# Kernel tuning notes

Hardware: AMD Instinct MI355X
Metric: run time of the kernel (lower is better)

Reference implementation:

```python
import jax, jax.numpy as jnp
import numpy as np

B, TQ, TKV, D_MODEL, H, DQ, DV = 4, 2048, 2048, 1024, 16, 64, 64
DK = DQ

def setup_inputs() -> dict:
    key = jax.random.key(0)
    ks = jax.random.split(key, 8)
    s = 0.02
    return {
        "query_sequence": jax.random.normal(ks[0], (B, TQ, D_MODEL), jnp.float32),
        "key_value_sequence": jax.random.normal(ks[1], (B, TKV, D_MODEL), jnp.float32),
        "key_value_padding_mask": jnp.zeros((B, TKV), dtype=bool),
        "Wq": jax.random.normal(ks[2], (D_MODEL, H * DQ), jnp.float32) * s,
        "bq": jnp.zeros((H * DQ,), jnp.float32),
        "Wkv": jax.random.normal(ks[3], (D_MODEL, H * (DK + DV)), jnp.float32) * s,
        "bkv": jnp.zeros((H * (DK + DV),), jnp.float32),
        "Wo": jax.random.normal(ks[4], (H * DV, D_MODEL), jnp.float32) * s,
        "bo": jnp.zeros((D_MODEL,), jnp.float32),
        "apply_causal_mask": 1,
    }

def reference(query_sequence, key_value_sequence, key_value_padding_mask,
              Wq, bq, Wkv, bkv, Wo, bo, apply_causal_mask):
    b, tq, _ = query_sequence.shape
    tkv = key_value_sequence.shape[1]
    q = (query_sequence @ Wq + bq).reshape(b, tq, H, DQ)          # (B,Tq,H,Dq)
    kv = key_value_sequence @ Wkv + bkv
    k = kv[..., : H * DK].reshape(b, tkv, H, DK)                   # (B,Tkv,H,Dk)
    v = kv[..., H * DK :].reshape(b, tkv, H, DV)                   # (B,Tkv,H,Dv)
    scores = jnp.einsum("bqhd,bkhd->bhqk", q, k) / jnp.sqrt(jnp.float32(DK))
    neg_inf = jnp.float32(-jnp.inf)
    scores = jnp.where(key_value_padding_mask[:, None, None, :], neg_inf, scores)
    if apply_causal_mask:
        causal = jnp.tril(jnp.ones((tq, tkv), dtype=bool))
        scores = jnp.where(causal[None, None, :, :], scores, neg_inf)
    attn = jax.nn.softmax(scores, axis=-1)
    out = jnp.einsum("bhqk,bkhd->bqhd", attn, v).reshape(b, tq, H * DV)
    return out @ Wo + bo
```

## Files before the change

kernel.cpp:

```cpp
#include <hip/hip_runtime.h>
#include <hip/hip_bf16.h>

#define B_   4
#define TQ_  2048
#define TKV_ 2048
#define DM_  1024
#define H_   16
#define DH_  64

#define SC_FOLD 0.18033688011112042f

using f32x4  = __attribute__((ext_vector_type(4))) float;
using f32x16 = __attribute__((ext_vector_type(16))) float;
using s16x8  = __attribute__((ext_vector_type(8))) short;

static __device__ __forceinline__ unsigned short f2bf(float f) {
  union { float f; unsigned int u; } v; v.f = f;
  unsigned int r = v.u + 0x7FFFu + ((v.u >> 16) & 1u);
  return (unsigned short)(r >> 16);
}
static __device__ __forceinline__ unsigned int pk2(float a, float b) {
  unsigned int r;
  asm("v_cvt_pk_bf16_f32 %0, %1, %2" : "=v"(r) : "v"(a), "v"(b));
  return r;
}
static __device__ __forceinline__ float max3f(float a, float b, float c) {
  float r;
  asm("v_max3_f32 %0, %1, %2, %3" : "=v"(r) : "v"(a), "v"(b), "v"(c));
  return r;
}

#define GL16(g, l)                                                          \
  __builtin_amdgcn_global_load_lds(                                         \
      (const __attribute__((address_space(1))) unsigned int*)(g),           \
      (__attribute__((address_space(3))) unsigned int*)(l), 16, 0, 0)

__global__ __launch_bounds__(256) void k_transpose_cast_all(
    const float* __restrict__ Wq, unsigned short* __restrict__ WqT,
    const float* __restrict__ Wkv, unsigned short* __restrict__ WkvT,
    const float* __restrict__ Wo, unsigned short* __restrict__ WoT) {
  __shared__ float t[64][65];
  int bid = blockIdx.x;
  const float* W;
  unsigned short* WT;
  int K = 1024, N, n0, k0;
  float scale;
  if (bid < 256) {
    W = Wq; WT = WqT; N = 1024; scale = SC_FOLD;
    n0 = (bid & 15) * 64; k0 = (bid >> 4) * 64;
  } else if (bid < 768) {
    int b2 = bid - 256;
    W = Wkv; WT = WkvT; N = 2048; scale = 1.0f;
    n0 = (b2 & 31) * 64; k0 = (b2 >> 5) * 64;
  } else {
    int b2 = bid - 768;
    W = Wo; WT = WoT; N = 1024; scale = 1.0f;
    n0 = (b2 & 15) * 64; k0 = (b2 >> 4) * 64;
  }
  int tx = threadIdx.x & 63, ty = threadIdx.x >> 6;
#pragma unroll
  for (int i = 0; i < 64; i += 4)
    t[ty + i][tx] = W[(size_t)(k0 + ty + i) * N + n0 + tx];
  __syncthreads();
#pragma unroll
  for (int i = 0; i < 64; i += 4)
    WT[(size_t)(n0 + ty + i) * K + k0 + tx] = f2bf(t[tx][ty + i] * scale);
}

__global__ __launch_bounds__(256) void k_cast_bf16(
    const float* __restrict__ in, unsigned short* __restrict__ out, int n4) {
  for (int i = blockIdx.x * 256 + threadIdx.x; i < n4; i += gridDim.x * 256) {
    f32x4 v = *(const f32x4*)(in + (size_t)i * 4);
    unsigned long long u = (unsigned long long)pk2(v[0], v[1]) |
                           ((unsigned long long)pk2(v[2], v[3]) << 32);
    *(unsigned long long*)(out + (size_t)i * 4) = u;
  }
}

template <int MODE, int BN>
__global__ __launch_bounds__(512, 2) void k_gemm8(
    const unsigned short* __restrict__ A, const unsigned short* __restrict__ BT,
    const float* __restrict__ bias, float bscale, unsigned short* __restrict__ out_a,
    unsigned short* __restrict__ out_b, float* __restrict__ out_f, int Kd) {
  constexpr int NI = BN / 64;
  constexpr int NH = NI / 2;
  __shared__ __align__(16) unsigned short As[2 * 256 * 64];
  __shared__ __align__(16) unsigned short Bs[2 * BN * 64];
  const int tid = threadIdx.x, lane = tid & 63, w = tid >> 6;
  const int wm = w >> 2, wn = w & 3;

  int nwg = gridDim.x * gridDim.y;
  int bid = blockIdx.y * gridDim.x + blockIdx.x;
  int cpx = nwg >> 3;
  int sw = (bid & 7) * cpx + (bid >> 3);
  int bx = sw % gridDim.x, by = sw / gridDim.x;
  int m0 = by * 256, n0 = bx * BN;

  const int strow = tid >> 3;
  const int sx = ((tid & 7) << 4) ^ ((strow & 7) << 4);
  const char* gA = (const char*)(A + (size_t)(m0 + strow) * Kd) + sx;
  const char* gB = (const char*)(BT + (size_t)(n0 + strow) * Kd) + sx;
  char* lA = (char*)As;
  char* lB = (char*)Bs;

#define ST_A(bf, c, k0) \
  GL16(gA + ((size_t)(c) * 64 * Kd + (size_t)(k0)) * 2, lA + (bf) * 32768 + (c) * 8192 + tid * 16)
#define ST_B(bf, c, k0) \
  GL16(gB + ((size_t)(c) * 64 * Kd + (size_t)(k0)) * 2, lB + (bf) * (BN * 128) + (c) * 8192 + tid * 16)

  f32x4 acc[8][NI];
#pragma unroll
  for (int i = 0; i < 8; ++i)
#pragma unroll
    for (int j = 0; j < NI; ++j) acc[i][j] = (f32x4){0.f, 0.f, 0.f, 0.f};

  s16x8 afr[4][2], bfr[NI][2];
  const int arow = wm * 128 + (lane & 15);
  const int brow = wn * (NI * 16) + (lane & 15);
  const int fcol = (lane >> 4) * 16;

#define RD_A(bf, r) (*(const s16x8*)(lA + (bf) * 32768 + (r) * 128 + ((fcol + _kk * 64) ^ (((r) & 7) << 4))))
#define RD_B(bf, r) (*(const s16x8*)(lB + (bf) * (BN * 128) + (r) * 128 + ((fcol + _kk * 64) ^ (((r) & 7) << 4))))

  const int nT = Kd >> 6;

  ST_B(0, 0, 0); ST_B(0, 1, 0);
  if (BN == 256) { ST_B(0, 2, 0); ST_B(0, 3, 0); }
  ST_A(0, 0, 0); ST_A(0, 2, 0);
  ST_A(0, 1, 0); ST_A(0, 3, 0);
  asm volatile("s_waitcnt vmcnt(2)" ::: "memory");
  __builtin_amdgcn_s_barrier();

#pragma unroll 1
  for (int t = 0; t < nT; ++t) {
    const int cur = t & 1, nxt = cur ^ 1;
    const int k1 = (t + 1) << 6;
    const bool st = (t + 1 < nT);

#pragma unroll
    for (int mi = 0; mi < 4; ++mi)
#pragma unroll
      for (int _kk = 0; _kk < 2; ++_kk) afr[mi][_kk] = RD_A(cur, arow + mi * 16);
#pragma unroll
    for (int ni = 0; ni < NH; ++ni)
#pragma unroll
      for (int _kk = 0; _kk < 2; ++_kk) bfr[ni][_kk] = RD_B(cur, brow + ni * 16);
    if (st) { ST_B(nxt, 0, k1); ST_B(nxt, 1, k1); }
    __builtin_amdgcn_s_barrier();
    __builtin_amdgcn_s_setprio(1);
#pragma unroll
    for (int mi = 0; mi < 4; ++mi)
#pragma unroll
      for (int ni = 0; ni < NH; ++ni)
#pragma unroll
        for (int kk = 0; kk < 2; ++kk)
          acc[mi][ni] = __builtin_amdgcn_mfma_f32_16x16x32_bf16(afr[mi][kk], bfr[ni][kk], acc[mi][ni], 0, 0, 0);
    __builtin_amdgcn_s_setprio(0);
    __builtin_amdgcn_s_barrier();

#pragma unroll
    for (int ni = NH; ni < NI; ++ni)
#pragma unroll
      for (int _kk = 0; _kk < 2; ++_kk) bfr[ni][_kk] = RD_B(cur, brow + ni * 16);
    if (st) {
      if (BN == 256) { ST_B(nxt, 2, k1); ST_B(nxt, 3, k1); }
      else           { ST_A(nxt, 0, k1); ST_A(nxt, 2, k1); }
    }
    if (st) asm volatile("s_waitcnt vmcnt(4)" ::: "memory");
    else    asm volatile("s_waitcnt vmcnt(0)" ::: "memory");
    __builtin_amdgcn_s_barrier();
    __builtin_amdgcn_s_setprio(1);
#pragma unroll
    for (int mi = 0; mi < 4; ++mi)
#pragma unroll
      for (int ni = NH; ni < NI; ++ni)
#pragma unroll
        for (int kk = 0; kk < 2; ++kk)
          acc[mi][ni] = __builtin_amdgcn_mfma_f32_16x16x32_bf16(afr[mi][kk], bfr[ni][kk], acc[mi][ni], 0, 0, 0);
    __builtin_amdgcn_s_setprio(0);
    __builtin_amdgcn_s_barrier();

#pragma unroll
    for (int mi = 0; mi < 4; ++mi)
#pragma unroll
      for (int _kk = 0; _kk < 2; ++_kk) afr[mi][_kk] = RD_A(cur, arow + (mi + 4) * 16);
    if (st) {
      if (BN == 256) { ST_A(nxt, 0, k1); ST_A(nxt, 2, k1); }
      else           { ST_A(nxt, 1, k1); ST_A(nxt, 3, k1); }
    }
    __builtin_amdgcn_s_barrier();
    __builtin_amdgcn_s_setprio(1);
#pragma unroll
    for (int mi = 0; mi < 4; ++mi)
#pragma unroll
      for (int ni = 0; ni < NH; ++ni)
#pragma unroll
        for (int kk = 0; kk < 2; ++kk)
          acc[mi + 4][ni] = __builtin_amdgcn_mfma_f32_16x16x32_bf16(afr[mi][kk], bfr[ni][kk], acc[mi + 4][ni], 0, 0, 0);
    __builtin_amdgcn_s_setprio(0);
    __builtin_amdgcn_s_barrier();

    if (st && BN == 256) { ST_A(nxt, 1, k1); ST_A(nxt, 3, k1); }
    asm volatile("s_waitcnt vmcnt(2)" ::: "memory");
    __builtin_amdgcn_s_barrier();
    __builtin_amdgcn_s_setprio(1);
#pragma unroll
    for (int mi = 0; mi < 4; ++mi)
#pragma unroll
      for (int ni = NH; ni < NI; ++ni)
#pragma unroll
        for (int kk = 0; kk < 2; ++kk)
          acc[mi + 4][ni] = __builtin_amdgcn_mfma_f32_16x16x32_bf16(afr[mi][kk], bfr[ni][kk], acc[mi + 4][ni], 0, 0, 0);
    __builtin_amdgcn_s_setprio(0);
    __builtin_amdgcn_s_barrier();
  }

#pragma unroll
  for (int mi = 0; mi < 8; ++mi) {
#pragma unroll
    for (int ni = 0; ni < NI; ++ni) {
      int col = n0 + wn * (NI * 16) + ni * 16 + (lane & 15);
      int rbase = m0 + wm * 128 + mi * 16 + (lane >> 4) * 4;
      float bv = bias[col] * bscale;
      if (MODE == 1 && col >= H_ * DH_) {
        int c2 = col - H_ * DH_;
        int h = c2 >> 6, d = c2 & 63;
        int b = rbase >> 11, tt = rbase & 2047;
        union { unsigned short h4[4]; unsigned long long u; } p;
#pragma unroll
        for (int r = 0; r < 4; ++r) p.h4[r] = f2bf(acc[mi][ni][r] + bv);
        *(unsigned long long*)(out_b + ((((size_t)b * H_ + h) * DH_ + d) * TKV_ + tt)) = p.u;
      } else {
#pragma unroll
        for (int r = 0; r < 4; ++r) {
          float v = acc[mi][ni][r] + bv;
          int m = rbase + r;
          if (MODE == 0) {
            int b = m >> 11, tt = m & 2047;
            int h = col >> 6, d = col & 63;
            out_a[(((size_t)b * H_ + h) * TQ_ + tt) * DH_ + d] = f2bf(v);
          } else if (MODE == 1) {
            int b = m >> 11, tt = m & 2047;
            int h = col >> 6, d = col & 63;
            out_a[(((size_t)b * H_ + h) * TKV_ + tt) * DH_ + d] = f2bf(v);
          } else {
            out_f[(size_t)m * DM_ + col] = v;
          }
        }
      }
    }
  }
#undef ST_A
#undef ST_B
#undef RD_A
#undef RD_B
}

__global__ __launch_bounds__(256, 2) void k_attn(
    const unsigned short* __restrict__ Qb, const unsigned short* __restrict__ Kb,
    const unsigned short* __restrict__ Vtb, const unsigned char* __restrict__ mask,
    const int* __restrict__ cflag, unsigned short* __restrict__ Ob) {
  __shared__ __align__(16) unsigned short Kt[2][128 * 64];
  __shared__ __align__(16) unsigned short Vt[2][64 * 128];
  __shared__ float bias_lds[2][128];
  __shared__ float red[4][32];
  __shared__ int s_any;

  int bid = blockIdx.y * gridDim.x + blockIdx.x;
  int r8 = bid & 7, q8 = bid >> 3;
  int bh = r8 * 8 + (q8 >> 3);
  int bx = q8 & 7;

  int b = bh >> 4, h = bh & 15;
  int tid = threadIdx.x, lane = tid & 63, w = tid >> 6;
  int hi = lane >> 5, l31 = lane & 31, l7 = lane & 7;
  const unsigned short* Qp = Qb + (size_t)bh * TQ_ * DH_;
  const char* Kp = (const char*)(Kb + (size_t)bh * TKV_ * DH_);
  const char* Vp = (const char*)(Vtb + (size_t)bh * DH_ * TKV_);
  const unsigned char* mp = mask + (size_t)b * TKV_;
  int causal = cflag[0];

  int st_r4 = tid >> 2;
  int st_c4 = (tid & 3) * 16;
  s16x8 pKr[4], pVr[4];

#define LOAD_KV(kv0)                                                          \
  {                                                                           \
    _Pragma("unroll")                                                         \
    for (int p = 0; p < 4; ++p) {                                             \
      int krow = (p >> 1) * 64 + st_r4;                                       \
      int kx = st_c4 + (p & 1) * 64;                                          \
      pKr[p] = *(const s16x8*)(Kp + ((size_t)((kv0) + krow) * 128 + kx));     \
      int vx = st_c4 + p * 64;                                                \
      pVr[p] = *(const s16x8*)(Vp + (((size_t)st_r4 * TKV_ + (kv0)) * 2 + vx)); \
    }                                                                         \
  }
#define WRITE_KV(bufi)                                                        \
  {                                                                           \
    char* kb_ = (char*)&Kt[bufi][0];                                          \
    char* vb_ = (char*)&Vt[bufi][0];                                          \
    _Pragma("unroll")                                                         \
    for (int p = 0; p < 4; ++p) {                                             \
      int krow = (p >> 1) * 64 + st_r4;                                       \
      int kx = st_c4 + (p & 1) * 64;                                          \
      *(s16x8*)(kb_ + krow * 128 + (kx ^ ((st_r4 & 7) << 4))) = pKr[p];       \
      int vx = st_c4 + p * 64;                                                \
      *(s16x8*)(vb_ + st_r4 * 256 + (vx ^ ((st_r4 & 7) << 4))) = pVr[p];      \
    }                                                                         \
  }

  if (tid == 0) s_any = 0;
  __syncthreads();
  {
    int any = 0;
    for (int i = tid; i < TKV_; i += 256) any |= mp[i];
    if (any) s_any = 1;
  }
  __syncthreads();
  const int has_mask = s_any;

#pragma unroll 1
  for (int pass = 0; pass < 2; ++pass) {
    int qb = (pass ? (15 - bx) : bx) * 128;
    int qw = qb + w * 32;
    int qrow = qw + l31;

    s16x8 bQ[4];
#pragma unroll
    for (int kk = 0; kk < 4; ++kk)
      bQ[kk] = *(const s16x8*)(Qp + (size_t)qrow * DH_ + kk * 16 + hi * 8);

    f32x16 accO[2];
#pragma unroll
    for (int i = 0; i < 16; ++i) { accO[0][i] = 0.f; accO[1][i] = 0.f; }
    float m_run = -INFINITY, l_run = 0.f;

    int nT = (causal ? (qb + 128) : TKV_) >> 7;

    LOAD_KV(0);
    WRITE_KV(0);
    if (has_mask && tid < 128) bias_lds[0][tid] = mp[tid] ? -1e30f : 0.0f;
    __syncthreads();

#pragma unroll 1
    for (int it = 0; it < nT; ++it) {
      int kv0 = it << 7;
      int cur = it & 1, nxt = cur ^ 1;
      if (it + 1 < nT) LOAD_KV(kv0 + 128);

      char* kbase = (char*)&Kt[cur][0];
      char* vbase = (char*)&Vt[cur][0];

      int nact = 4;
      if (causal) {
        int rem = qw + 31 - kv0;
        nact = rem < 0 ? 0 : ((rem >> 5) + 1);
        if (nact > 4) nact = 4;
      }

      if (nact > 0) {
        f32x16 sT[4];
        __builtin_amdgcn_s_setprio(1);
#pragma unroll
        for (int s = 0; s < 4; ++s) {
          if (s < nact) {
#pragma unroll
            for (int i = 0; i < 16; ++i) sT[s][i] = 0.f;
#pragma unroll
            for (int kk = 0; kk < 4; ++kk) {
              s16x8 aK = *(const s16x8*)(kbase + (s * 32 + l31) * 128 +
                                         ((kk * 32 + hi * 16) ^ (l7 << 4)));
              sT[s] = __builtin_amdgcn_mfma_f32_32x32x16_bf16(aK, bQ[kk], sT[s], 0, 0, 0);
            }
          }
        }
        __builtin_amdgcn_s_setprio(0);

        float a0 = -INFINITY, a1 = -INFINITY, a2 = -INFINITY, a3 = -INFINITY;
#pragma unroll
        for (int s = 0; s < 4; ++s) {
          if (s < nact) {
            int diag_s = causal && (kv0 + s * 32 + 31 > qw);
            if (diag_s || has_mask) {
#pragma unroll
              for (int r = 0; r < 16; ++r) {
                int kvloc = s * 32 + (r & 3) + 8 * (r >> 2) + 4 * hi;
                float sv = sT[s][r];
                if (has_mask) sv += bias_lds[cur][kvloc];
                if (diag_s && (kv0 + kvloc) > qrow) sv = -1e30f;
                sT[s][r] = sv;
              }
            }
#pragma unroll
            for (int r = 0; r < 16; r += 4) {
              a0 = fmaxf(a0, sT[s][r + 0]); a1 = fmaxf(a1, sT[s][r + 1]);
              a2 = fmaxf(a2, sT[s][r + 2]); a3 = fmaxf(a3, sT[s][r + 3]);
            }
          }
        }
        float mx = max3f(max3f(a0, a1, a2), a3, -3.0e30f);
        mx = fmaxf(mx, __shfl_xor(mx, 32));

        if (!__all(mx - m_run <= 8.0f)) {
          float mnew = fmaxf(m_run, mx);
          float sc_o = exp2f(m_run - mnew);
          m_run = mnew;
          l_run *= sc_o;
          red[w][l31] = sc_o;
#pragma unroll
          for (int r = 0; r < 16; ++r) {
            float f = red[w][(r & 3) + 8 * (r >> 2) + 4 * hi];
            accO[0][r] *= f;
            accO[1][r] *= f;
          }
        }

        float s0acc = 0.f, s1acc = 0.f, s2acc = 0.f, s3acc = 0.f;
#pragma unroll
        for (int s = 0; s < 4; ++s) {
          if (s < nact) {
#pragma unroll
            for (int r = 0; r < 16; r += 4) {
              float p0 = exp2f(sT[s][r + 0] - m_run);
              float p1 = exp2f(sT[s][r + 1] - m_run);
              float p2 = exp2f(sT[s][r + 2] - m_run);
              float p3 = exp2f(sT[s][r + 3] - m_run);
              sT[s][r + 0] = p0; sT[s][r + 1] = p1;
              sT[s][r + 2] = p2; sT[s][r + 3] = p3;
              s0acc += p0; s1acc += p1; s2acc += p2; s3acc += p3;
            }
          }
        }
        float ls = (s0acc + s1acc) + (s2acc + s3acc);
        ls += __shfl_xor(ls, 32);
        l_run += ls;

#pragma unroll
        for (int c = 0; c < 8; ++c) {
          if ((c >> 1) < nact) {
            int s = c >> 1, kk = c & 1;
            unsigned int x0 = pk2(sT[s][8 * kk + 0], sT[s][8 * kk + 1]);
            unsigned int y0 = pk2(sT[s][8 * kk + 2], sT[s][8 * kk + 3]);
            unsigned int x1 = pk2(sT[s][8 * kk + 4], sT[s][8 * kk + 5]);
            unsigned int y1 = pk2(sT[s][8 * kk + 6], sT[s][8 * kk + 7]);
            asm("v_permlane32_swap_b32 %0, %1" : "+v"(x0), "+v"(x1));
            asm("v_permlane32_swap_b32 %0, %1" : "+v"(y0), "+v"(y1));
            union { unsigned int u[4]; s16x8 v; } pf;
            pf.u[0] = x0;
            pf.u[1] = y0;
            pf.u[2] = x1;
            pf.u[3] = y1;
            __builtin_amdgcn_s_setprio(1);
#pragma unroll
            for (int dt = 0; dt < 2; ++dt) {
              s16x8 vf = *(const s16x8*)(vbase + (dt * 32 + l31) * 256 +
                                         ((c * 32 + hi * 16) ^ (l7 << 4)));
              accO[dt] = __builtin_amdgcn_mfma_f32_32x32x16_bf16(pf.v, vf, accO[dt], 0, 0, 0);
            }
            __builtin_amdgcn_s_setprio(0);
          }
        }
      }

      if (it + 1 < nT) {
        WRITE_KV(nxt);
        if (has_mask && tid < 128) bias_lds[nxt][tid] = mp[kv0 + 128 + tid] ? -1e30f : 0.0f;
      }
      __syncthreads();
    }

    red[w][l31] = 1.0f / l_run;
#pragma unroll
    for (int r = 0; r < 16; ++r) {
      int R = (r & 3) + 8 * (r >> 2) + 4 * hi;
      float f = red[w][R];
      int qg = qw + R;
      size_t base = ((size_t)b * TQ_ + qg) * DM_ + h * DH_ + l31;
      Ob[base] = f2bf(accO[0][r] * f);
      Ob[base + 32] = f2bf(accO[1][r] * f);
    }
  }
#undef LOAD_KV
#undef WRITE_KV
}

extern "C" void kernel_launch(void* const* d_in, const int* in_sizes, int n_in,
                              void* d_out, int out_size, void* d_ws, size_t ws_size,
                              hipStream_t stream) {
  const float* xq  = (const float*)d_in[0];
  const float* xkv = (const float*)d_in[1];
  const unsigned char* mask = (const unsigned char*)d_in[2];
  const float* Wq  = (const float*)d_in[3];
  const float* bq  = (const float*)d_in[4];
  const float* Wkv = (const float*)d_in[5];
  const float* bkv = (const float*)d_in[6];
  const float* Wo  = (const float*)d_in[7];
  const float* bo  = (const float*)d_in[8];
  const int* cflag = (const int*)d_in[9];
  float* out = (float*)d_out;

  char* ws = (char*)d_ws;
  unsigned short* WqT  = (unsigned short*)(ws);
  unsigned short* WkvT = (unsigned short*)(ws + ((size_t)2 << 20));
  unsigned short* WoT  = (unsigned short*)(ws + ((size_t)6 << 20));
  unsigned short* Qb   = (unsigned short*)(ws + ((size_t)8 << 20));
  unsigned short* Kb   = (unsigned short*)(ws + ((size_t)24 << 20));
  unsigned short* Vb   = (unsigned short*)(ws + ((size_t)40 << 20));
  unsigned short* Xr   = (unsigned short*)(ws + ((size_t)56 << 20));
  unsigned short* Ob   = Xr;

  k_transpose_cast_all<<<1024, 256, 0, stream>>>(Wq, WqT, Wkv, WkvT, Wo, WoT);

  k_cast_bf16<<<2048, 256, 0, stream>>>(xq, Xr, B_ * TQ_ * DM_ / 4);
  k_gemm8<0, 128><<<dim3(8, 32), 512, 0, stream>>>(Xr, WqT, bq, SC_FOLD, Qb, nullptr, nullptr, 1024);

  k_cast_bf16<<<2048, 256, 0, stream>>>(xkv, Xr, B_ * TKV_ * DM_ / 4);
  k_gemm8<1, 256><<<dim3(8, 32), 512, 0, stream>>>(Xr, WkvT, bkv, 1.0f, Kb, Vb, nullptr, 1024);

  k_attn<<<dim3(8, B_ * H_), 256, 0, stream>>>(Qb, Kb, Vb, mask, cflag, Ob);

  k_gemm8<2, 128><<<dim3(8, 32), 512, 0, stream>>>(Ob, WoT, bo, 1.0f, nullptr, nullptr, out, 1024);
}
```

Baseline: 191.6 us.

## Widen attention blocks to 512 threads covering 256 query rows per tile

Changes the attention kernel from 4 to 8 waves per block, so each block handles 256 query rows per pass and the grid halves to 4x64 blocks. K/V tiles staged in shared memory are now shared by twice as many query rows, which halves global K/V traffic per query, and the per-thread load work is split over more threads. The trade-offs are fewer blocks in flight, coarser causal load balancing across the paired passes, and tighter launch bounds that may limit registers.

```diff
diff --git a/kernel.cpp b/kernel.cpp
--- a/kernel.cpp
+++ b/kernel.cpp
@@ -256,20 +256,20 @@
 #undef RD_B
 }
 
-__global__ __launch_bounds__(256, 2) void k_attn(
+__global__ __launch_bounds__(512, 4) void k_attn(
     const unsigned short* __restrict__ Qb, const unsigned short* __restrict__ Kb,
     const unsigned short* __restrict__ Vtb, const unsigned char* __restrict__ mask,
     const int* __restrict__ cflag, unsigned short* __restrict__ Ob) {
   __shared__ __align__(16) unsigned short Kt[2][128 * 64];
   __shared__ __align__(16) unsigned short Vt[2][64 * 128];
   __shared__ float bias_lds[2][128];
-  __shared__ float red[4][32];
+  __shared__ float red[8][32];
   __shared__ int s_any;
 
   int bid = blockIdx.y * gridDim.x + blockIdx.x;
   int r8 = bid & 7, q8 = bid >> 3;
-  int bh = r8 * 8 + (q8 >> 3);
-  int bx = q8 & 7;
+  int bh = r8 * 8 + (q8 >> 2);
+  int bx = q8 & 3;
 
   int b = bh >> 4, h = bh & 15;
   int tid = threadIdx.x, lane = tid & 63, w = tid >> 6;
@@ -280,40 +280,34 @@
   const unsigned char* mp = mask + (size_t)b * TKV_;
   int causal = cflag[0];
 
-  int st_r4 = tid >> 2;
-  int st_c4 = (tid & 3) * 16;
-  s16x8 pKr[4], pVr[4];
+  int st_kr = tid >> 2;
+  int st_kc = (tid & 3) * 16;
+  int st_vr = tid >> 3;
+  int st_vc = (tid & 7) * 16;
+  s16x8 pKr[2], pVr[2];
 
 #define LOAD_KV(kv0)                                                          \
   {                                                                           \
-    _Pragma("unroll")                                                         \
-    for (int p = 0; p < 4; ++p) {                                             \
-      int krow = (p >> 1) * 64 + st_r4;                                       \
-      int kx = st_c4 + (p & 1) * 64;                                          \
-      pKr[p] = *(const s16x8*)(Kp + ((size_t)((kv0) + krow) * 128 + kx));     \
-      int vx = st_c4 + p * 64;                                                \
-      pVr[p] = *(const s16x8*)(Vp + (((size_t)st_r4 * TKV_ + (kv0)) * 2 + vx)); \
-    }                                                                         \
+    pKr[0] = *(const s16x8*)(Kp + ((size_t)((kv0) + st_kr) * 128 + st_kc));   \
+    pKr[1] = *(const s16x8*)(Kp + ((size_t)((kv0) + st_kr) * 128 + st_kc + 64)); \
+    pVr[0] = *(const s16x8*)(Vp + (((size_t)st_vr * TKV_ + (kv0)) * 2 + st_vc)); \
+    pVr[1] = *(const s16x8*)(Vp + (((size_t)st_vr * TKV_ + (kv0)) * 2 + st_vc + 128)); \
   }
 #define WRITE_KV(bufi)                                                        \
   {                                                                           \
     char* kb_ = (char*)&Kt[bufi][0];                                          \
     char* vb_ = (char*)&Vt[bufi][0];                                          \
-    _Pragma("unroll")                                                         \
-    for (int p = 0; p < 4; ++p) {                                             \
-      int krow = (p >> 1) * 64 + st_r4;                                       \
-      int kx = st_c4 + (p & 1) * 64;                                          \
-      *(s16x8*)(kb_ + krow * 128 + (kx ^ ((st_r4 & 7) << 4))) = pKr[p];       \
-      int vx = st_c4 + p * 64;                                                \
-      *(s16x8*)(vb_ + st_r4 * 256 + (vx ^ ((st_r4 & 7) << 4))) = pVr[p];      \
-    }                                                                         \
+    *(s16x8*)(kb_ + st_kr * 128 + (st_kc ^ ((st_kr & 7) << 4))) = pKr[0];     \
+    *(s16x8*)(kb_ + st_kr * 128 + ((st_kc + 64) ^ ((st_kr & 7) << 4))) = pKr[1]; \
+    *(s16x8*)(vb_ + st_vr * 256 + (st_vc ^ ((st_vr & 7) << 4))) = pVr[0];     \
+    *(s16x8*)(vb_ + st_vr * 256 + ((st_vc + 128) ^ ((st_vr & 7) << 4))) = pVr[1]; \
   }
 
   if (tid == 0) s_any = 0;
   __syncthreads();
   {
     int any = 0;
-    for (int i = tid; i < TKV_; i += 256) any |= mp[i];
+    for (int i = tid; i < TKV_; i += 512) any |= mp[i];
     if (any) s_any = 1;
   }
   __syncthreads();
@@ -321,7 +315,7 @@
 
 #pragma unroll 1
   for (int pass = 0; pass < 2; ++pass) {
-    int qb = (pass ? (15 - bx) : bx) * 128;
+    int qb = (pass ? (7 - bx) : bx) * 256;
     int qw = qb + w * 32;
     int qrow = qw + l31;
 
@@ -335,7 +329,7 @@
     for (int i = 0; i < 16; ++i) { accO[0][i] = 0.f; accO[1][i] = 0.f; }
     float m_run = -INFINITY, l_run = 0.f;
 
-    int nT = (causal ? (qb + 128) : TKV_) >> 7;
+    int nT = (causal ? (qb + 256) : TKV_) >> 7;
 
     LOAD_KV(0);
     WRITE_KV(0);
@@ -517,7 +511,7 @@
   k_cast_bf16<<<2048, 256, 0, stream>>>(xkv, Xr, B_ * TKV_ * DM_ / 4);
   k_gemm8<1, 256><<<dim3(8, 32), 512, 0, stream>>>(Xr, WkvT, bkv, 1.0f, Kb, Vb, nullptr, 1024);
 
-  k_attn<<<dim3(8, B_ * H_), 256, 0, stream>>>(Qb, Kb, Vb, mask, cflag, Ob);
+  k_attn<<<dim3(4, B_ * H_), 512, 0, stream>>>(Qb, Kb, Vb, mask, cflag, Ob);
 
   k_gemm8<2, 128><<<dim3(8, 32), 512, 0, stream>>>(Ob, WoT, bo, 1.0f, nullptr, nullptr, out, 1024);
 }
```

Measured after the change: 355.1 us. 1.85x slower.

## Merge weight prep with input casts and fuse Q and KV projection GEMMs

Applied to the files above, without the earlier changes.

Merges the weight transposes and both activation casts into one prep kernel, and runs the Q and KV projection GEMMs as a single launch with 512 workgroups. This removes launch gaps and serialization between small kernels and lets the Q and KV GEMMs share the GPU at once. KV activations need a separate workspace region, so the fused path only runs when the workspace is large enough; otherwise it falls back to separate launches. The fused GEMM reserves LDS sized for BN=256 even for Q blocks, which could change occupancy.

```diff
diff --git a/kernel.cpp b/kernel.cpp
--- a/kernel.cpp
+++ b/kernel.cpp
@@ -35,28 +35,9 @@
       (const __attribute__((address_space(1))) unsigned int*)(g),           \
       (__attribute__((address_space(3))) unsigned int*)(l), 16, 0, 0)
 
-__global__ __launch_bounds__(256) void k_transpose_cast_all(
-    const float* __restrict__ Wq, unsigned short* __restrict__ WqT,
-    const float* __restrict__ Wkv, unsigned short* __restrict__ WkvT,
-    const float* __restrict__ Wo, unsigned short* __restrict__ WoT) {
-  __shared__ float t[64][65];
-  int bid = blockIdx.x;
-  const float* W;
-  unsigned short* WT;
-  int K = 1024, N, n0, k0;
-  float scale;
-  if (bid < 256) {
-    W = Wq; WT = WqT; N = 1024; scale = SC_FOLD;
-    n0 = (bid & 15) * 64; k0 = (bid >> 4) * 64;
-  } else if (bid < 768) {
-    int b2 = bid - 256;
-    W = Wkv; WT = WkvT; N = 2048; scale = 1.0f;
-    n0 = (b2 & 31) * 64; k0 = (b2 >> 5) * 64;
-  } else {
-    int b2 = bid - 768;
-    W = Wo; WT = WoT; N = 1024; scale = 1.0f;
-    n0 = (b2 & 15) * 64; k0 = (b2 >> 4) * 64;
-  }
+static __device__ __forceinline__ void transpose_tile(
+    const float* W, unsigned short* WT, int K, int N, int n0, int k0, float scale,
+    float (*t)[65]) {
   int tx = threadIdx.x & 63, ty = threadIdx.x >> 6;
 #pragma unroll
   for (int i = 0; i < 64; i += 4)
@@ -66,10 +47,9 @@
   for (int i = 0; i < 64; i += 4)
     WT[(size_t)(n0 + ty + i) * K + k0 + tx] = f2bf(t[tx][ty + i] * scale);
 }
-
-__global__ __launch_bounds__(256) void k_cast_bf16(
-    const float* __restrict__ in, unsigned short* __restrict__ out, int n4) {
-  for (int i = blockIdx.x * 256 + threadIdx.x; i < n4; i += gridDim.x * 256) {
+static __device__ __forceinline__ void cast_gs(
+    const float* in, unsigned short* out, int n4, int cb, int ncb) {
+  for (int i = cb * 256 + threadIdx.x; i < n4; i += ncb * 256) {
     f32x4 v = *(const f32x4*)(in + (size_t)i * 4);
     unsigned long long u = (unsigned long long)pk2(v[0], v[1]) |
                            ((unsigned long long)pk2(v[2], v[3]) << 32);
@@ -77,23 +57,42 @@
   }
 }
 
+__global__ __launch_bounds__(256) void k_prep(
+    const float* __restrict__ Wq, unsigned short* __restrict__ WqT,
+    const float* __restrict__ Wkv, unsigned short* __restrict__ WkvT,
+    const float* __restrict__ Wo, unsigned short* __restrict__ WoT,
+    const float* __restrict__ xq, unsigned short* __restrict__ Aq,
+    const float* __restrict__ xkv, unsigned short* __restrict__ Akv, int n4) {
+  int bid = blockIdx.x;
+  if (bid >= 3072) { cast_gs(xkv, Akv, n4, bid - 3072, 2048); return; }
+  if (bid >= 1024) { cast_gs(xq, Aq, n4, bid - 1024, 2048); return; }
+  __shared__ float t[64][65];
+  if (bid < 256) {
+    transpose_tile(Wq, WqT, 1024, 1024, (bid & 15) * 64, (bid >> 4) * 64, SC_FOLD, t);
+  } else if (bid < 768) {
+    int b2 = bid - 256;
+    transpose_tile(Wkv, WkvT, 1024, 2048, (b2 & 31) * 64, (b2 >> 5) * 64, 1.0f, t);
+  } else {
+    int b2 = bid - 768;
+    transpose_tile(Wo, WoT, 1024, 1024, (b2 & 15) * 64, (b2 >> 4) * 64, 1.0f, t);
+  }
+}
+
+__global__ __launch_bounds__(256) void k_cast_bf16(
+    const float* __restrict__ in, unsigned short* __restrict__ out, int n4) {
+  cast_gs(in, out, n4, blockIdx.x, gridDim.x);
+}
+
 template <int MODE, int BN>
-__global__ __launch_bounds__(512, 2) void k_gemm8(
+static __device__ __forceinline__ void gemm_body(
     const unsigned short* __restrict__ A, const unsigned short* __restrict__ BT,
     const float* __restrict__ bias, float bscale, unsigned short* __restrict__ out_a,
-    unsigned short* __restrict__ out_b, float* __restrict__ out_f, int Kd) {
+    unsigned short* __restrict__ out_b, float* __restrict__ out_f, int Kd,
+    int bx, int by, unsigned short* As, unsigned short* Bs) {
   constexpr int NI = BN / 64;
   constexpr int NH = NI / 2;
-  __shared__ __align__(16) unsigned short As[2 * 256 * 64];
-  __shared__ __align__(16) unsigned short Bs[2 * BN * 64];
   const int tid = threadIdx.x, lane = tid & 63, w = tid >> 6;
   const int wm = w >> 2, wn = w & 3;
-
-  int nwg = gridDim.x * gridDim.y;
-  int bid = blockIdx.y * gridDim.x + blockIdx.x;
-  int cpx = nwg >> 3;
-  int sw = (bid & 7) * cpx + (bid >> 3);
-  int bx = sw % gridDim.x, by = sw / gridDim.x;
   int m0 = by * 256, n0 = bx * BN;
 
   const int strow = tid >> 3;
@@ -256,6 +255,41 @@
 #undef RD_B
 }
 
+template <int MODE, int BN>
+__global__ __launch_bounds__(512, 2) void k_gemm8(
+    const unsigned short* __restrict__ A, const unsigned short* __restrict__ BT,
+    const float* __restrict__ bias, float bscale, unsigned short* __restrict__ out_a,
+    unsigned short* __restrict__ out_b, float* __restrict__ out_f, int Kd) {
+  __shared__ __align__(16) unsigned short As[2 * 256 * 64];
+  __shared__ __align__(16) unsigned short Bs[2 * BN * 64];
+  int nwg = gridDim.x * gridDim.y;
+  int bid = blockIdx.y * gridDim.x + blockIdx.x;
+  int cpx = nwg >> 3;
+  int sw = (bid & 7) * cpx + (bid >> 3);
+  int bx = sw % gridDim.x, by = sw / gridDim.x;
+  gemm_body<MODE, BN>(A, BT, bias, bscale, out_a, out_b, out_f, Kd, bx, by, As, Bs);
+}
+
+__global__ __launch_bounds__(512, 2) void k_gemm_qkv(
+    const unsigned short* __restrict__ Aq, const unsigned short* __restrict__ WqT,
+    const float* __restrict__ bq,
+    const unsigned short* __restrict__ Akv, const unsigned short* __restrict__ WkvT,
+    const float* __restrict__ bkv,
+    unsigned short* __restrict__ Qb, unsigned short* __restrict__ Kb,
+    unsigned short* __restrict__ Vb) {
+  __shared__ __align__(16) unsigned short As[2 * 256 * 64];
+  __shared__ __align__(16) unsigned short Bs[2 * 256 * 64];
+  bool isQ = blockIdx.y < 32;
+  int lby = isQ ? blockIdx.y : (blockIdx.y - 32);
+  int bid = lby * 8 + blockIdx.x;
+  int sw = (bid & 7) * 32 + (bid >> 3);
+  int bx = sw & 7, by = sw >> 3;
+  if (isQ)
+    gemm_body<0, 128>(Aq, WqT, bq, SC_FOLD, Qb, nullptr, nullptr, 1024, bx, by, As, Bs);
+  else
+    gemm_body<1, 256>(Akv, WkvT, bkv, 1.0f, Kb, Vb, nullptr, 1024, bx, by, As, Bs);
+}
+
 __global__ __launch_bounds__(256, 2) void k_attn(
     const unsigned short* __restrict__ Qb, const unsigned short* __restrict__ Kb,
     const unsigned short* __restrict__ Vtb, const unsigned char* __restrict__ mask,
@@ -508,16 +542,20 @@
   unsigned short* Vb   = (unsigned short*)(ws + ((size_t)40 << 20));
   unsigned short* Xr   = (unsigned short*)(ws + ((size_t)56 << 20));
   unsigned short* Ob   = Xr;
-
-  k_transpose_cast_all<<<1024, 256, 0, stream>>>(Wq, WqT, Wkv, WkvT, Wo, WoT);
-
-  k_cast_bf16<<<2048, 256, 0, stream>>>(xq, Xr, B_ * TQ_ * DM_ / 4);
-  k_gemm8<0, 128><<<dim3(8, 32), 512, 0, stream>>>(Xr, WqT, bq, SC_FOLD, Qb, nullptr, nullptr, 1024);
-
-  k_cast_bf16<<<2048, 256, 0, stream>>>(xkv, Xr, B_ * TKV_ * DM_ / 4);
-  k_gemm8<1, 256><<<dim3(8, 32), 512, 0, stream>>>(Xr, WkvT, bkv, 1.0f, Kb, Vb, nullptr, 1024);
-
-  k_attn<<<dim3(8, B_ * H_), 256, 0, stream>>>(Qb, Kb, Vb, mask, cflag, Ob);
-
-  k_gemm8<2, 128><<<dim3(8, 32), 512, 0, stream>>>(Ob, WoT, bo, 1.0f, nullptr, nullptr, out, 1024);
-}
+  const int n4 = B_ * TQ_ * DM_ / 4;
+
+  if (ws_size >= ((size_t)88 << 20)) {
+    unsigned short* Akv = (unsigned short*)(ws + ((size_t)72 << 20));
+    k_prep<<<5120, 256, 0, stream>>>(Wq, WqT, Wkv, WkvT, Wo, WoT, xq, Xr, xkv, Akv, n4);
+    k_gemm_qkv<<<dim3(8, 64), 512, 0, stream>>>(Xr, WqT, bq, Akv, WkvT, bkv, Qb, Kb, Vb);
+    k_attn<<<dim3(8, B_ * H_), 256, 0, stream>>>(Qb, Kb, Vb, mask, cflag, Ob);
+    k_gemm8<2, 128><<<dim3(8, 32), 512, 0, stream>>>(Ob, WoT, bo, 1.0f, nullptr, nullptr, out, 1024);
+  } else {
+    k_prep<<<3072, 256, 0, stream>>>(Wq, WqT, Wkv, WkvT, Wo, WoT, xq, Xr, xkv, nullptr, n4);
+    k_gemm8<0, 128><<<dim3(8, 32), 512, 0, stream>>>(Xr, WqT, bq, SC_FOLD, Qb, nullptr, nullptr, 1024);
+    k_cast_bf16<<<2048, 256, 0, stream>>>(xkv, Xr, n4);
+    k_gemm8<1, 256><<<dim3(8, 32), 512, 0, stream>>>(Xr, WkvT, bkv, 1.0f, Kb, Vb, nullptr, 1024);
+    k_attn<<<dim3(8, B_ * H_), 256, 0, stream>>>(Qb, Kb, Vb, mask, cflag, Ob);
+    k_gemm8<2, 128><<<dim3(8, 32), 512, 0, stream>>>(Ob, WoT, bo, 1.0f, nullptr, nullptr, out, 1024);
+  }
+}
```

Measured after the change: 183.8 us, median of 2. 1.04x faster.
